# Performance work log

Measured on AMD Instinct MI355X. Metric: run time of the kernel, lower is better.

Reference implementation:

```python
import jax, jax.numpy as jnp
import numpy as np

B, T, N, H, W, C = 2, 3, 6, 256, 704, 17  # raster_shape=(256,704), 17 nuScenes classes
P = 500_000  # total supervised pixels across all (batch, time, camera) buckets


def setup_inputs() -> dict:
    key = jax.random.key(0)
    k1, k2, k3, k4, k5 = jax.random.split(key, 5)
    values = jax.random.normal(k1, (B, T, N, H, W, C), jnp.float32)
    idx_b = jax.random.randint(k2, (P,), 0, B)
    idx_t = jax.random.randint(k3, (P,), 0, T)
    idx_n = jax.random.randint(k4, (P,), 0, N)
    indices = jnp.stack([idx_b, idx_t, idx_n], axis=1).astype(jnp.int32)  # [P,3]
    # coors are (row, col) pixel coordinates in [0,H) x [0,W)
    coors = jax.random.uniform(k5, (P, 2), jnp.float32) * jnp.array([H, W], jnp.float32)
    return {"values": values, "indices": indices, "coors": coors}


def reference(values, indices, coors):
    # Faithful, fused version of GaussianFlowOccRasterizer.sample_indices:
    # the padded bucketize -> grid_sample -> re-gather pipeline equals direct
    # per-point bilinear sampling of image flat_idx[p] at pixel (coors[p]-0.5)
    # (grid_sample align_corners=False, padding_mode='zeros'); padded rows are
    # discarded by the final gather so they never affect the result.
    Bv, Tv, Nv, Hv, Wv, Cv = values.shape
    imgs = values.reshape(Bv * Tv * Nv, Hv, Wv, Cv)
    flat = indices[:, 0] * (Tv * Nv) + indices[:, 1] * Nv + indices[:, 2]  # [P]

    # grid = (coors[..., [1,0]] / [W, H]) * 2 - 1; unnormalized (align_corners=False):
    # pix = ((grid + 1) * size - 1) / 2  ==  coor - 0.5
    ix = coors[:, 1] - 0.5
    iy = coors[:, 0] - 0.5
    x0 = jnp.floor(ix)
    y0 = jnp.floor(iy)
    wx = ix - x0  # [P]
    wy = iy - y0
    x0i = x0.astype(jnp.int32)
    y0i = y0.astype(jnp.int32)

    def corner(xc, yc):
        inb = (xc >= 0) & (xc < Wv) & (yc >= 0) & (yc < Hv)
        v = imgs[flat, jnp.clip(yc, 0, Hv - 1), jnp.clip(xc, 0, Wv - 1)]  # [P,C]
        return jnp.where(inb[:, None], v, jnp.zeros((), values.dtype))

    v00 = corner(x0i, y0i)
    v01 = corner(x0i + 1, y0i)
    v10 = corner(x0i, y0i + 1)
    v11 = corner(x0i + 1, y0i + 1)

    wx = wx[:, None]
    wy = wy[:, None]
    out = (v00 * (1 - wx) * (1 - wy) + v01 * wx * (1 - wy)
           + v10 * (1 - wx) * wy + v11 * wx * wy)  # [P,C]
    return out
```

## Files before the change

kernel.cpp:

```cpp
#include <hip/hip_runtime.h>

#define B_ 2
#define T_ 3
#define N_ 6
#define H_ 256
#define W_ 704
#define C_ 17
#define P_ 500000

__global__ __launch_bounds__(256) void bilerp_gather_kernel(
    const float* __restrict__ values,
    const int*   __restrict__ indices,
    const float* __restrict__ coors,
    float*       __restrict__ out)
{
    const int tid  = threadIdx.x;
    const int wave = blockIdx.x * (blockDim.x >> 6) + (tid >> 6);
    const int lane = tid & 63;
    const int sub  = lane / 17;
    const int c    = lane - sub * 17;
    const int p    = wave * 3 + sub;
    if (sub >= 3 || p >= P_) return;

    const int ib = indices[p * 3 + 0];
    const int it = indices[p * 3 + 1];
    const int in = indices[p * 3 + 2];
    const int flat = (ib * T_ + it) * N_ + in;

    const float iy = coors[p * 2 + 0] - 0.5f;
    const float ix = coors[p * 2 + 1] - 0.5f;
    const float x0f = floorf(ix);
    const float y0f = floorf(iy);
    const float wx = ix - x0f;
    const float wy = iy - y0f;
    const int x0 = (int)x0f;
    const int y0 = (int)y0f;
    const int x1 = x0 + 1;
    const int y1 = y0 + 1;

    const int x0c = min(max(x0, 0), W_ - 1);
    const int x1c = min(max(x1, 0), W_ - 1);
    const int y0c = min(max(y0, 0), H_ - 1);
    const int y1c = min(max(y1, 0), H_ - 1);

    const float* __restrict__ img = values + (size_t)flat * (H_ * W_ * C_);

    const float v00 = img[((size_t)y0c * W_ + x0c) * C_ + c];
    const float v01 = img[((size_t)y0c * W_ + x1c) * C_ + c];
    const float v10 = img[((size_t)y1c * W_ + x0c) * C_ + c];
    const float v11 = img[((size_t)y1c * W_ + x1c) * C_ + c];

    const bool xin0 = (x0 >= 0) & (x0 < W_);
    const bool xin1 = (x1 >= 0) & (x1 < W_);
    const bool yin0 = (y0 >= 0) & (y0 < H_);
    const bool yin1 = (y1 >= 0) & (y1 < H_);

    float w00 = (1.f - wx) * (1.f - wy);
    float w01 = wx * (1.f - wy);
    float w10 = (1.f - wx) * wy;
    float w11 = wx * wy;
    w00 = (xin0 & yin0) ? w00 : 0.f;
    w01 = (xin1 & yin0) ? w01 : 0.f;
    w10 = (xin0 & yin1) ? w10 : 0.f;
    w11 = (xin1 & yin1) ? w11 : 0.f;

    const float r = v00 * w00 + v01 * w01 + v10 * w10 + v11 * w11;
    __builtin_nontemporal_store(r, &out[(size_t)p * C_ + c]);
}

extern "C" void kernel_launch(void* const* d_in, const int* in_sizes, int n_in,
                              void* d_out, int out_size, void* d_ws, size_t ws_size,
                              hipStream_t stream)
{
    const float* values  = (const float*)d_in[0];
    const int*   indices = (const int*)d_in[1];
    const float* coors   = (const float*)d_in[2];
    float* out = (float*)d_out;

    const int block = 256;
    const int points_per_block = 12;
    const int grid = (P_ + points_per_block - 1) / points_per_block;

    bilerp_gather_kernel<<<grid, block, 0, stream>>>(values, indices, coors, out);
}
```

Before: 50.71 us.

## Bin sample points by image and row band before bilinear gather

```diff
diff --git a/kernel.cpp b/kernel.cpp
--- a/kernel.cpp
+++ b/kernel.cpp
@@ -8,10 +8,71 @@
 #define C_ 17
 #define P_ 500000
 
+#define NIMG   (B_ * T_ * N_)
+#define BANDS  64
+#define NBINS  (NIMG * BANDS)
+
+__global__ __launch_bounds__(256) void bin_kernel(
+    const int*   __restrict__ indices,
+    const float* __restrict__ coors,
+    int* __restrict__ binOf,
+    int* __restrict__ counts)
+{
+    int p = blockIdx.x * blockDim.x + threadIdx.x;
+    if (p >= P_) return;
+    int ib = indices[p * 3 + 0];
+    int it = indices[p * 3 + 1];
+    int in = indices[p * 3 + 2];
+    int flat = (ib * T_ + it) * N_ + in;
+    float iy = coors[p * 2 + 0] - 0.5f;
+    int y0 = (int)floorf(iy);
+    int band = min(max(y0, 0), H_ - 1) >> 2;
+    int b = flat * BANDS + band;
+    binOf[p] = b;
+    atomicAdd(&counts[b], 1);
+}
+
+__global__ __launch_bounds__(256) void scan_kernel(int* __restrict__ counts)
+{
+    __shared__ int buf[256];
+    const int t = threadIdx.x;
+    const int base = t * (NBINS / 256);
+    int local[NBINS / 256];
+    int s = 0;
+    #pragma unroll
+    for (int i = 0; i < NBINS / 256; ++i) { local[i] = counts[base + i]; s += local[i]; }
+    buf[t] = s;
+    __syncthreads();
+    int inc = s;
+    for (int off = 1; off < 256; off <<= 1) {
+        int v = (t >= off) ? buf[t - off] : 0;
+        __syncthreads();
+        buf[t] += v;
+        inc = buf[t];
+        __syncthreads();
+    }
+    int run = inc - s;
+    #pragma unroll
+    for (int i = 0; i < NBINS / 256; ++i) { counts[base + i] = run; run += local[i]; }
+}
+
+__global__ __launch_bounds__(256) void scatter_kernel(
+    const int* __restrict__ binOf,
+    int* __restrict__ cursor,
+    int* __restrict__ order)
+{
+    int p = blockIdx.x * blockDim.x + threadIdx.x;
+    if (p >= P_) return;
+    int pos = atomicAdd(&cursor[binOf[p]], 1);
+    order[pos] = p;
+}
+
+template<bool SORTED>
 __global__ __launch_bounds__(256) void bilerp_gather_kernel(
     const float* __restrict__ values,
     const int*   __restrict__ indices,
     const float* __restrict__ coors,
+    const int*   __restrict__ order,
     float*       __restrict__ out)
 {
     const int tid  = threadIdx.x;
@@ -19,8 +80,9 @@
     const int lane = tid & 63;
     const int sub  = lane / 17;
     const int c    = lane - sub * 17;
-    const int p    = wave * 3 + sub;
-    if (sub >= 3 || p >= P_) return;
+    const int pidx = wave * 3 + sub;
+    if (sub >= 3 || pidx >= P_) return;
+    const int p = SORTED ? order[pidx] : pidx;
 
     const int ib = indices[p * 3 + 0];
     const int it = indices[p * 3 + 1];
@@ -79,7 +141,22 @@
 
     const int block = 256;
     const int points_per_block = 12;
-    const int grid = (P_ + points_per_block - 1) / points_per_block;
+    const int gather_grid = (P_ + points_per_block - 1) / points_per_block;
+    const int pt_grid = (P_ + block - 1) / block;
 
-    bilerp_gather_kernel<<<grid, block, 0, stream>>>(values, indices, coors, out);
+    const size_t ws_need = (size_t)(NBINS + 2 * P_) * sizeof(int);
+    if (ws_size >= ws_need) {
+        int* counts = (int*)d_ws;
+        int* binOf  = counts + NBINS;
+        int* order  = binOf + P_;
+        hipMemsetAsync(counts, 0, NBINS * sizeof(int), stream);
+        bin_kernel<<<pt_grid, block, 0, stream>>>(indices, coors, binOf, counts);
+        scan_kernel<<<1, 256, 0, stream>>>(counts);
+        scatter_kernel<<<pt_grid, block, 0, stream>>>(binOf, counts, order);
+        bilerp_gather_kernel<true><<<gather_grid, block, 0, stream>>>(
+            values, indices, coors, order, out);
+    } else {
+        bilerp_gather_kernel<false><<<gather_grid, block, 0, stream>>>(
+            values, indices, coors, nullptr, out);
+    }
 }
```

Result: slower. 192.3 us (+279.2%).
